# Kernel optimization log

Measured on AMD Instinct MI355X. Metric: run time of the kernel, lower is better.

Reference implementation:

```python
import jax, jax.numpy as jnp
import numpy as np

B, L, H = 16, 2048, 768
V, D = 30000, 64


def setup_inputs() -> dict:
    key = jax.random.key(0)
    k1, k2, k3, k4 = jax.random.split(key, 4)
    bert_x = jax.random.normal(k1, (B, L, H), dtype=jnp.float32)
    x = jax.random.randint(k2, (B, L), 0, V, dtype=jnp.int64)
    ae = jax.random.normal(k3, (V, D), dtype=jnp.float32)
    w = jax.random.normal(k4, (D, D), dtype=jnp.float32)
    return {"bert_x": bert_x, "x": x, "ae": ae, "w": w}


def reference(bert_x, x, ae, w):
    # E[b,i] = ae[x[b,i]]  -> [B, L, D]
    E = ae[x]
    # fac[b,i,j] = E[b,i] @ w @ E[b,j]   (bilinear pairwise score)
    scores = jnp.einsum('bid,de,bje->bij', E, w, E)
    Lseq = bert_x.shape[1]
    i = jnp.arange(Lseq, dtype=bert_x.dtype)[:, None]
    j = jnp.arange(Lseq, dtype=bert_x.dtype)[None, :]
    # strictly-causal weight (i+1)/(j+1) for i < j, zero elsewhere
    coef = jnp.where(i < j, (i + 1.0) / (j + 1.0), 0.0).astype(bert_x.dtype)
    # res[:, j] = bert_x[:, j] + sum_{i<j} bert_x[:, i] * coef[i,j] * fac[b,i,j]
    res = bert_x + jnp.einsum('bij,bih->bjh', scores * coef, bert_x)
    return res
```

## Files before the change

kernel.cpp:

```cpp
#include <hip/hip_runtime.h>

#define Bb 16
#define Ll 2048
#define Hh 768
#define Dd 64
#define Cc 64
#define HC 48
#define NT (Hh / HC)
#define NCH (Ll / Cc)

typedef __attribute__((ext_vector_type(8))) short bf16x8;
typedef __attribute__((ext_vector_type(4))) float f32x4;

__device__ __forceinline__ short f2bf(float f) {
  union { float f; unsigned u; } c;
  c.f = f;
  unsigned r = (c.u + 0x7FFFu + ((c.u >> 16) & 1u)) >> 16;
  return (short)r;
}
__device__ __forceinline__ unsigned pack2(float a, float b) {
  return (unsigned)(unsigned short)f2bf(a) | ((unsigned)(unsigned short)f2bf(b) << 16);
}

__device__ __forceinline__ void sync_lds() {
  asm volatile("s_waitcnt lgkmcnt(0)\n\ts_barrier" ::: "memory");
}

__global__ __launch_bounds__(256) void prep_kernel(const int* __restrict__ x,
                                                   const float* __restrict__ ae,
                                                   const float* __restrict__ w,
                                                   short* __restrict__ Eg,
                                                   short* __restrict__ FTg,
                                                   short* __restrict__ scTg) {
  const int tid = threadIdx.x;
  const int wv = tid >> 6, lane = tid & 63, quad = lane >> 4, lq = lane & 15;
  const int b = blockIdx.x >> 5, ch = blockIdx.x & 31;
  const size_t gb = (size_t)blockIdx.x * 4096;
  __shared__ short sE[64 * 64];
  __shared__ short sWT[64 * 64];
  __shared__ short sF[64 * 64];

  {
    const int i = tid >> 2, seg = tid & 3;
    const int idx = x[b * Ll + ch * Cc + i];
    const float4* aer = (const float4*)(ae + (size_t)idx * Dd) + seg * 4;
    float4 ev[4];
#pragma unroll
    for (int q = 0; q < 4; ++q) ev[q] = aer[q];
    uint4 pA, pB;
    pA.x = pack2(ev[0].x, ev[0].y); pA.y = pack2(ev[0].z, ev[0].w);
    pA.z = pack2(ev[1].x, ev[1].y); pA.w = pack2(ev[1].z, ev[1].w);
    pB.x = pack2(ev[2].x, ev[2].y); pB.y = pack2(ev[2].z, ev[2].w);
    pB.z = pack2(ev[3].x, ev[3].y); pB.w = pack2(ev[3].z, ev[3].w);
    *(uint4*)&sE[i * 64 + (((2 * seg) ^ (i & 7)) << 3)] = pA;
    *(uint4*)&sE[i * 64 + (((2 * seg + 1) ^ (i & 7)) << 3)] = pB;
    *(uint4*)(Eg + gb + i * 64 + seg * 16) = pA;
    *(uint4*)(Eg + gb + i * 64 + seg * 16 + 8) = pB;
    const float4* wr = (const float4*)w;
#pragma unroll
    for (int q = 0; q < 4; ++q) {
      const int fl = q * 256 + tid;
      const int d = fl >> 4, es = (fl & 15) * 4;
      const float4 v = wr[fl];
      const float vv[4] = {v.x, v.y, v.z, v.w};
#pragma unroll
      for (int c = 0; c < 4; ++c) {
        const int e = es + c;
        sWT[e * 64 + (((d >> 3) ^ (e & 7)) << 3) + (d & 7)] = f2bf(vv[c]);
      }
    }
  }
  __syncthreads();

  const int rm = wv * 16 + lq;
  bf16x8 aE[2], aW[2];
#pragma unroll
  for (int ks = 0; ks < 2; ++ks) {
    const int blk = ((ks * 4 + quad) ^ (rm & 7)) << 3;
    aE[ks] = *(const bf16x8*)&sE[rm * 64 + blk];
    aW[ks] = *(const bf16x8*)&sWT[rm * 64 + blk];
  }

#pragma unroll
  for (int nt = 0; nt < 4; ++nt) {
    const int rn = nt * 16 + lq;
    f32x4 accF = {}, accT = {};
#pragma unroll
    for (int ks = 0; ks < 2; ++ks) {
      const int blk = ((ks * 4 + quad) ^ (rn & 7)) << 3;
      const bf16x8 bW = *(const bf16x8*)&sWT[rn * 64 + blk];
      const bf16x8 bE = *(const bf16x8*)&sE[rn * 64 + blk];
      accF = __builtin_amdgcn_mfma_f32_16x16x32_bf16(aE[ks], bW, accF, 0, 0, 0);
      accT = __builtin_amdgcn_mfma_f32_16x16x32_bf16(aW[ks], bE, accT, 0, 0, 0);
    }
#pragma unroll
    for (int r = 0; r < 4; ++r) {
      const int i = wv * 16 + quad * 4 + r;
      const int e = nt * 16 + lq;
      sF[i * 64 + (((e >> 3) ^ (i & 7)) << 3) + (e & 7)] = f2bf(accF[r]);
      const int e2 = wv * 16 + quad * 4 + r;
      const int i2 = nt * 16 + lq;
      FTg[gb + e2 * 64 + i2] = f2bf(accT[r]);
    }
  }
  __syncthreads();

#pragma unroll
  for (int nt = 0; nt < 4; ++nt) {
    const int rn = nt * 16 + lq;
    f32x4 acc = {};
#pragma unroll
    for (int ks = 0; ks < 2; ++ks) {
      const int blk = ((ks * 4 + quad) ^ (rn & 7)) << 3;
      const bf16x8 bF = *(const bf16x8*)&sF[rn * 64 + blk];
      acc = __builtin_amdgcn_mfma_f32_16x16x32_bf16(aE[ks], bF, acc, 0, 0, 0);
    }
#pragma unroll
    for (int r = 0; r < 4; ++r) {
      const int j = wv * 16 + quad * 4 + r;
      const int i = nt * 16 + lq;
      scTg[gb + j * 64 + i] = f2bf(i < j ? acc[r] : 0.f);
    }
  }
}

__global__ __launch_bounds__(256) void scan_kernel(const float* __restrict__ bx,
                                                   const short* __restrict__ Eg,
                                                   const short* __restrict__ FTg,
                                                   const short* __restrict__ scTg,
                                                   float* __restrict__ out) {
  const int tile = blockIdx.x;
  const int b = blockIdx.y;
  const int tid = threadIdx.x;
  const int w = tid >> 6, lane = tid & 63, quad = lane >> 4, lq = lane & 15;

  __shared__ short sE[64 * 64];
  __shared__ short sSc[64 * 64];
  __shared__ short sFT[64 * 64];
  __shared__ short sGT[48 * 64];
  __shared__ short sST[48 * 64];

  f32x4 accS[3] = {};
  uint4 rE[2], rS[2], rF[2];
  float2 rG[6];
  float rB[12];

  const int ip = tid & 31, hg = tid >> 5;

  auto load_chunk = [&](int ch) {
    const size_t tb = (size_t)(b * NCH + ch) * 4096;
    const uint4* gE = (const uint4*)(Eg + tb);
    const uint4* gS = (const uint4*)(scTg + tb);
    const uint4* gF = (const uint4*)(FTg + tb);
#pragma unroll
    for (int t2 = 0; t2 < 2; ++t2) {
      const int idx = t2 * 256 + tid;
      rE[t2] = gE[idx];
      rS[t2] = gS[idx];
      rF[t2] = gF[idx];
    }
    const int p0 = ch * Cc;
    const float* xr = bx + ((size_t)(b * Ll) + p0 + 2 * ip) * Hh + tile * HC + hg * 6;
#pragma unroll
    for (int k = 0; k < 3; ++k) {
      rG[k] = *(const float2*)(xr + 2 * k);
      rG[3 + k] = *(const float2*)(xr + Hh + 2 * k);
    }
    const float* br = bx + ((size_t)(b * Ll) + p0 + w * 16 + quad * 4) * Hh + tile * HC + lq;
#pragma unroll
    for (int ht = 0; ht < 3; ++ht)
#pragma unroll
      for (int r = 0; r < 4; ++r) rB[ht * 4 + r] = br[(size_t)r * Hh + ht * 16];
  };

  load_chunk(0);

  for (int ch = 0; ch < NCH; ++ch) {
    const int p0 = ch * Cc;
    sync_lds();

#pragma unroll
    for (int t2 = 0; t2 < 2; ++t2) {
      const int idx = t2 * 256 + tid;
      const int r_ = idx >> 3, bl = idx & 7;
      const int dst = r_ * 64 + ((bl ^ (r_ & 7)) << 3);
      *(uint4*)&sE[dst] = rE[t2];
      *(uint4*)&sSc[dst] = rS[t2];
      *(uint4*)&sFT[dst] = rF[t2];
    }
    {
      const float s0 = (float)(p0 + 2 * ip + 1), s1 = (float)(p0 + 2 * ip + 2);
#pragma unroll
      for (int k = 0; k < 3; ++k) {
#pragma unroll
        for (int c = 0; c < 2; ++c) {
          const int h = hg * 6 + 2 * k + c;
          const float g0 = (c ? rG[k].y : rG[k].x) * s0;
          const float g1 = (c ? rG[3 + k].y : rG[3 + k].x) * s1;
          const int sa = h * 64 + (((ip >> 2) ^ (h & 7)) << 3) + 2 * (ip & 3);
          *(unsigned*)&sGT[sa] = pack2(g0, g1);
        }
      }
    }
#pragma unroll
    for (int ht = 0; ht < 3; ++ht)
#pragma unroll
      for (int r = 0; r < 4; ++r) {
        const int h = ht * 16 + quad * 4 + r;
        const int d = w * 16 + lq;
        sST[h * 64 + (((d >> 3) ^ (h & 7)) << 3) + (d & 7)] = f2bf(accS[ht][r]);
      }

    float myB[12];
#pragma unroll
    for (int q = 0; q < 12; ++q) myB[q] = rB[q];
    load_chunk(ch + 1 < NCH ? ch + 1 : NCH - 1);

    sync_lds();

    f32x4 accO[3] = {};
    {
      const int rj = w * 16 + lq;
      bf16x8 aC1[2], aC2[2], bD[2];
#pragma unroll
      for (int ks = 0; ks < 2; ++ks) {
        const int blk = ((ks * 4 + quad) ^ (rj & 7)) << 3;
        aC1[ks] = *(const bf16x8*)(sSc + rj * 64 + blk);
        aC2[ks] = *(const bf16x8*)(sE + rj * 64 + blk);
        bD[ks] = *(const bf16x8*)(sFT + rj * 64 + blk);
      }
#pragma unroll
      for (int ht = 0; ht < 3; ++ht) {
        const int rh = ht * 16 + lq;
#pragma unroll
        for (int ks = 0; ks < 2; ++ks) {
          const int blk = ((ks * 4 + quad) ^ (rh & 7)) << 3;
          bf16x8 g = *(const bf16x8*)(sGT + rh * 64 + blk);
          bf16x8 st = *(const bf16x8*)(sST + rh * 64 + blk);
          accO[ht] = __builtin_amdgcn_mfma_f32_16x16x32_bf16(aC1[ks], g, accO[ht], 0, 0, 0);
          accO[ht] = __builtin_amdgcn_mfma_f32_16x16x32_bf16(aC2[ks], st, accO[ht], 0, 0, 0);
          accS[ht] = __builtin_amdgcn_mfma_f32_16x16x32_bf16(g, bD[ks], accS[ht], 0, 0, 0);
        }
      }
    }

#pragma unroll
    for (int ht = 0; ht < 3; ++ht) {
#pragma unroll
      for (int r = 0; r < 4; ++r) {
        const int gj = p0 + w * 16 + quad * 4 + r;
        const size_t off = ((size_t)(b * Ll) + gj) * Hh + tile * HC + ht * 16 + lq;
        out[off] = myB[ht * 4 + r] + accO[ht][r] * (1.0f / (float)(gj + 1));
      }
    }
  }
}

extern "C" void kernel_launch(void* const* d_in, const int* in_sizes, int n_in,
                              void* d_out, int out_size, void* d_ws, size_t ws_size,
                              hipStream_t stream) {
  (void)in_sizes; (void)n_in; (void)out_size; (void)ws_size;
  const float* bx = (const float*)d_in[0];
  const int* x = (const int*)d_in[1];
  const float* ae = (const float*)d_in[2];
  const float* w = (const float*)d_in[3];
  float* out = (float*)d_out;
  short* Eg = (short*)d_ws;
  short* FTg = Eg + (size_t)512 * 4096;
  short* scTg = FTg + (size_t)512 * 4096;

  prep_kernel<<<Bb * NCH, 256, 0, stream>>>(x, ae, w, Eg, FTg, scTg);
  dim3 grid(NT, Bb);
  scan_kernel<<<grid, 256, 0, stream>>>(bx, Eg, FTg, scTg, out);
}
```

Before: 256.2 us.

## Split sequence scan into parallel segments with precomputed per-segment state prefix

```diff
diff --git a/kernel.cpp b/kernel.cpp
--- a/kernel.cpp
+++ b/kernel.cpp
@@ -5,9 +5,12 @@
 #define Hh 768
 #define Dd 64
 #define Cc 64
-#define HC 48
+#define HC 64
 #define NT (Hh / HC)
 #define NCH (Ll / Cc)
+#define PSEG 8
+#define CPS (NCH / PSEG)
+#define NHT (HC / 16)
 
 typedef __attribute__((ext_vector_type(8))) short bf16x8;
 typedef __attribute__((ext_vector_type(4))) float f32x4;
@@ -20,6 +23,11 @@
 }
 __device__ __forceinline__ unsigned pack2(float a, float b) {
   return (unsigned)(unsigned short)f2bf(a) | ((unsigned)(unsigned short)f2bf(b) << 16);
+}
+__device__ __forceinline__ float bf2f(short s) {
+  union { unsigned u; float f; } c;
+  c.u = ((unsigned)(unsigned short)s) << 16;
+  return c.f;
 }
 
 __device__ __forceinline__ void sync_lds() {
@@ -124,135 +132,187 @@
   }
 }
 
+__global__ __launch_bounds__(256) void state_kernel(const float* __restrict__ bx,
+                                                    const short* __restrict__ FTg,
+                                                    short* __restrict__ Sg) {
+  const int tile = blockIdx.x, b = blockIdx.y, seg = blockIdx.z;
+  const int tid = threadIdx.x;
+  const int w = tid >> 6, lane = tid & 63, quad = lane >> 4, lq = lane & 15;
+  const int ip = tid & 31, hg = tid >> 5;
+  const int rj = w * 16 + lq;
+
+  __shared__ short sGT[2][HC * 64];
+
+  f32x4 accS[NHT] = {};
+  float2 rG[2 * NHT];
+  bf16x8 bD[2];
+
+  auto load_G = [&](int ch) {
+    const float* xr = bx + ((size_t)(b * Ll) + ch * Cc + 2 * ip) * Hh + tile * HC + hg * 8;
+#pragma unroll
+    for (int k = 0; k < NHT; ++k) {
+      rG[k] = *(const float2*)(xr + 2 * k);
+      rG[NHT + k] = *(const float2*)(xr + Hh + 2 * k);
+    }
+  };
+  auto load_D = [&](int ch) {
+    const size_t tb = (size_t)(b * NCH + ch) * 4096;
+#pragma unroll
+    for (int ks = 0; ks < 2; ++ks)
+      bD[ks] = *(const bf16x8*)(FTg + tb + rj * 64 + (ks * 4 + quad) * 8);
+  };
+
+  load_G(seg * CPS);
+  load_D(seg * CPS);
+
+#pragma unroll
+  for (int c = 0; c < CPS; ++c) {
+    const int ch = seg * CPS + c;
+    const int cur = c & 1;
+    const int p0 = ch * Cc;
+    {
+      const float s0 = (float)(p0 + 2 * ip + 1), s1 = (float)(p0 + 2 * ip + 2);
+#pragma unroll
+      for (int k = 0; k < NHT; ++k)
+#pragma unroll
+        for (int cc = 0; cc < 2; ++cc) {
+          const int h = hg * 8 + 2 * k + cc;
+          const float g0 = (cc ? rG[k].y : rG[k].x) * s0;
+          const float g1 = (cc ? rG[NHT + k].y : rG[NHT + k].x) * s1;
+          const int sa = h * 64 + (((ip >> 2) ^ (h & 7)) << 3) + 2 * (ip & 3);
+          *(unsigned*)&sGT[cur][sa] = pack2(g0, g1);
+        }
+    }
+    if (c + 1 < CPS) load_G(ch + 1);
+    sync_lds();
+#pragma unroll
+    for (int ht = 0; ht < NHT; ++ht) {
+      const int rh = ht * 16 + lq;
+#pragma unroll
+      for (int ks = 0; ks < 2; ++ks) {
+        const int blk = ((ks * 4 + quad) ^ (rh & 7)) << 3;
+        const bf16x8 g = *(const bf16x8*)&sGT[cur][rh * 64 + blk];
+        accS[ht] = __builtin_amdgcn_mfma_f32_16x16x32_bf16(g, bD[ks], accS[ht], 0, 0, 0);
+      }
+    }
+    if (c + 1 < CPS) load_D(ch + 1);
+  }
+
+  short* Sr = Sg + (size_t)(b * (PSEG - 1) + seg) * (Hh * 64);
+#pragma unroll
+  for (int ht = 0; ht < NHT; ++ht)
+#pragma unroll
+    for (int r = 0; r < 4; ++r) {
+      const int h = tile * HC + ht * 16 + quad * 4 + r;
+      Sr[h * 64 + w * 16 + lq] = f2bf(accS[ht][r]);
+    }
+}
+
 __global__ __launch_bounds__(256) void scan_kernel(const float* __restrict__ bx,
                                                    const short* __restrict__ Eg,
                                                    const short* __restrict__ FTg,
                                                    const short* __restrict__ scTg,
+                                                   const short* __restrict__ Sg,
                                                    float* __restrict__ out) {
-  const int tile = blockIdx.x;
-  const int b = blockIdx.y;
+  const int tile = blockIdx.x, b = blockIdx.y, seg = blockIdx.z;
   const int tid = threadIdx.x;
   const int w = tid >> 6, lane = tid & 63, quad = lane >> 4, lq = lane & 15;
-
-  __shared__ short sE[64 * 64];
-  __shared__ short sSc[64 * 64];
-  __shared__ short sFT[64 * 64];
-  __shared__ short sGT[48 * 64];
-  __shared__ short sST[48 * 64];
-
-  f32x4 accS[3] = {};
-  uint4 rE[2], rS[2], rF[2];
-  float2 rG[6];
-  float rB[12];
-
   const int ip = tid & 31, hg = tid >> 5;
-
-  auto load_chunk = [&](int ch) {
+  const int rj = w * 16 + lq;
+
+  __shared__ short sGT[2][HC * 64];
+  __shared__ short sST[2][HC * 64];
+
+  f32x4 accS[NHT] = {};
+  bf16x8 aC1[2], aC2[2], bD[2];
+  float2 rG[2 * NHT];
+
+  auto load_G = [&](int ch) {
+    const float* xr = bx + ((size_t)(b * Ll) + ch * Cc + 2 * ip) * Hh + tile * HC + hg * 8;
+#pragma unroll
+    for (int k = 0; k < NHT; ++k) {
+      rG[k] = *(const float2*)(xr + 2 * k);
+      rG[NHT + k] = *(const float2*)(xr + Hh + 2 * k);
+    }
+  };
+  auto load_frag = [&](int ch) {
     const size_t tb = (size_t)(b * NCH + ch) * 4096;
-    const uint4* gE = (const uint4*)(Eg + tb);
-    const uint4* gS = (const uint4*)(scTg + tb);
-    const uint4* gF = (const uint4*)(FTg + tb);
-#pragma unroll
-    for (int t2 = 0; t2 < 2; ++t2) {
-      const int idx = t2 * 256 + tid;
-      rE[t2] = gE[idx];
-      rS[t2] = gS[idx];
-      rF[t2] = gF[idx];
-    }
+#pragma unroll
+    for (int ks = 0; ks < 2; ++ks) {
+      const int o = rj * 64 + (ks * 4 + quad) * 8;
+      aC1[ks] = *(const bf16x8*)(scTg + tb + o);
+      aC2[ks] = *(const bf16x8*)(Eg + tb + o);
+      bD[ks]  = *(const bf16x8*)(FTg + tb + o);
+    }
+  };
+
+  load_G(seg * CPS);
+  load_frag(seg * CPS);
+
+  for (int s = 0; s < seg; ++s) {
+    const short* Sr = Sg + (size_t)(b * (PSEG - 1) + s) * (Hh * 64);
+#pragma unroll
+    for (int ht = 0; ht < NHT; ++ht)
+#pragma unroll
+      for (int r = 0; r < 4; ++r) {
+        const int h = tile * HC + ht * 16 + quad * 4 + r;
+        accS[ht][r] += bf2f(Sr[h * 64 + w * 16 + lq]);
+      }
+  }
+
+#pragma unroll
+  for (int c = 0; c < CPS; ++c) {
+    const int ch = seg * CPS + c;
+    const int cur = c & 1;
     const int p0 = ch * Cc;
-    const float* xr = bx + ((size_t)(b * Ll) + p0 + 2 * ip) * Hh + tile * HC + hg * 6;
-#pragma unroll
-    for (int k = 0; k < 3; ++k) {
-      rG[k] = *(const float2*)(xr + 2 * k);
-      rG[3 + k] = *(const float2*)(xr + Hh + 2 * k);
-    }
-    const float* br = bx + ((size_t)(b * Ll) + p0 + w * 16 + quad * 4) * Hh + tile * HC + lq;
-#pragma unroll
-    for (int ht = 0; ht < 3; ++ht)
-#pragma unroll
-      for (int r = 0; r < 4; ++r) rB[ht * 4 + r] = br[(size_t)r * Hh + ht * 16];
-  };
-
-  load_chunk(0);
-
-  for (int ch = 0; ch < NCH; ++ch) {
-    const int p0 = ch * Cc;
-    sync_lds();
-
-#pragma unroll
-    for (int t2 = 0; t2 < 2; ++t2) {
-      const int idx = t2 * 256 + tid;
-      const int r_ = idx >> 3, bl = idx & 7;
-      const int dst = r_ * 64 + ((bl ^ (r_ & 7)) << 3);
-      *(uint4*)&sE[dst] = rE[t2];
-      *(uint4*)&sSc[dst] = rS[t2];
-      *(uint4*)&sFT[dst] = rF[t2];
-    }
     {
       const float s0 = (float)(p0 + 2 * ip + 1), s1 = (float)(p0 + 2 * ip + 2);
 #pragma unroll
-      for (int k = 0; k < 3; ++k) {
-#pragma unroll
-        for (int c = 0; c < 2; ++c) {
-          const int h = hg * 6 + 2 * k + c;
-          const float g0 = (c ? rG[k].y : rG[k].x) * s0;
-          const float g1 = (c ? rG[3 + k].y : rG[3 + k].x) * s1;
+      for (int k = 0; k < NHT; ++k)
+#pragma unroll
+        for (int cc = 0; cc < 2; ++cc) {
+          const int h = hg * 8 + 2 * k + cc;
+          const float g0 = (cc ? rG[k].y : rG[k].x) * s0;
+          const float g1 = (cc ? rG[NHT + k].y : rG[NHT + k].x) * s1;
           const int sa = h * 64 + (((ip >> 2) ^ (h & 7)) << 3) + 2 * (ip & 3);
-          *(unsigned*)&sGT[sa] = pack2(g0, g1);
+          *(unsigned*)&sGT[cur][sa] = pack2(g0, g1);
         }
-      }
-    }
-#pragma unroll
-    for (int ht = 0; ht < 3; ++ht)
+    }
+#pragma unroll
+    for (int ht = 0; ht < NHT; ++ht)
 #pragma unroll
       for (int r = 0; r < 4; ++r) {
         const int h = ht * 16 + quad * 4 + r;
         const int d = w * 16 + lq;
-        sST[h * 64 + (((d >> 3) ^ (h & 7)) << 3) + (d & 7)] = f2bf(accS[ht][r]);
-      }
-
-    float myB[12];
-#pragma unroll
-    for (int q = 0; q < 12; ++q) myB[q] = rB[q];
-    load_chunk(ch + 1 < NCH ? ch + 1 : NCH - 1);
-
+        sST[cur][h * 64 + (((d >> 3) ^ (h & 7)) << 3) + (d & 7)] = f2bf(accS[ht][r]);
+      }
+    if (c + 1 < CPS) load_G(ch + 1);
     sync_lds();
 
-    f32x4 accO[3] = {};
-    {
-      const int rj = w * 16 + lq;
-      bf16x8 aC1[2], aC2[2], bD[2];
+    f32x4 accO[NHT] = {};
+#pragma unroll
+    for (int ht = 0; ht < NHT; ++ht) {
+      const int rh = ht * 16 + lq;
 #pragma unroll
       for (int ks = 0; ks < 2; ++ks) {
-        const int blk = ((ks * 4 + quad) ^ (rj & 7)) << 3;
-        aC1[ks] = *(const bf16x8*)(sSc + rj * 64 + blk);
-        aC2[ks] = *(const bf16x8*)(sE + rj * 64 + blk);
-        bD[ks] = *(const bf16x8*)(sFT + rj * 64 + blk);
-      }
-#pragma unroll
-      for (int ht = 0; ht < 3; ++ht) {
-        const int rh = ht * 16 + lq;
-#pragma unroll
-        for (int ks = 0; ks < 2; ++ks) {
-          const int blk = ((ks * 4 + quad) ^ (rh & 7)) << 3;
-          bf16x8 g = *(const bf16x8*)(sGT + rh * 64 + blk);
-          bf16x8 st = *(const bf16x8*)(sST + rh * 64 + blk);
-          accO[ht] = __builtin_amdgcn_mfma_f32_16x16x32_bf16(aC1[ks], g, accO[ht], 0, 0, 0);
-          accO[ht] = __builtin_amdgcn_mfma_f32_16x16x32_bf16(aC2[ks], st, accO[ht], 0, 0, 0);
-          accS[ht] = __builtin_amdgcn_mfma_f32_16x16x32_bf16(g, bD[ks], accS[ht], 0, 0, 0);
-        }
-      }
-    }
-
-#pragma unroll
-    for (int ht = 0; ht < 3; ++ht) {
+        const int blk = ((ks * 4 + quad) ^ (rh & 7)) << 3;
+        const bf16x8 g  = *(const bf16x8*)&sGT[cur][rh * 64 + blk];
+        const bf16x8 st = *(const bf16x8*)&sST[cur][rh * 64 + blk];
+        accO[ht] = __builtin_amdgcn_mfma_f32_16x16x32_bf16(aC1[ks], g,  accO[ht], 0, 0, 0);
+        accO[ht] = __builtin_amdgcn_mfma_f32_16x16x32_bf16(aC2[ks], st, accO[ht], 0, 0, 0);
+        accS[ht] = __builtin_amdgcn_mfma_f32_16x16x32_bf16(g, bD[ks],  accS[ht], 0, 0, 0);
+      }
+    }
+    if (c + 1 < CPS) load_frag(ch + 1);
+
+#pragma unroll
+    for (int ht = 0; ht < NHT; ++ht)
 #pragma unroll
       for (int r = 0; r < 4; ++r) {
         const int gj = p0 + w * 16 + quad * 4 + r;
         const size_t off = ((size_t)(b * Ll) + gj) * Hh + tile * HC + ht * 16 + lq;
-        out[off] = myB[ht * 4 + r] + accO[ht][r] * (1.0f / (float)(gj + 1));
-      }
-    }
+        out[off] = bx[off] + accO[ht][r] * (1.0f / (float)(gj + 1));
+      }
   }
 }
 
@@ -268,8 +328,11 @@
   short* Eg = (short*)d_ws;
   short* FTg = Eg + (size_t)512 * 4096;
   short* scTg = FTg + (size_t)512 * 4096;
+  short* Sg = scTg + (size_t)512 * 4096;
 
   prep_kernel<<<Bb * NCH, 256, 0, stream>>>(x, ae, w, Eg, FTg, scTg);
-  dim3 grid(NT, Bb);
-  scan_kernel<<<grid, 256, 0, stream>>>(bx, Eg, FTg, scTg, out);
-}
+  dim3 gst(NT, Bb, PSEG - 1);
+  state_kernel<<<gst, 256, 0, stream>>>(bx, FTg, Sg);
+  dim3 gsc(NT, Bb, PSEG);
+  scan_kernel<<<gsc, 256, 0, stream>>>(bx, Eg, FTg, scTg, Sg, out);
+}
```

Result: no change. 254.0 us (-0.9%).
